# Kernel tuning notes

Measured on AMD Instinct MI355X. Metric: run time of the kernel, lower is better.

## Reference

```python
import jax, jax.numpy as jnp
import numpy as np

N_NODES = 100000
N_EDGES = 1600000
IN_CH = 128
OUT_CH = 64

def setup_inputs() -> dict:
    key = jax.random.key(0)
    k = jax.random.split(key, 7)
    x = jax.random.normal(k[0], (N_NODES, IN_CH), dtype=jnp.float32)
    edge_index = jax.random.randint(k[1], (2, N_EDGES), 0, N_NODES, dtype=jnp.int64)
    neg_edge_index = jax.random.randint(k[2], (2, N_EDGES), 0, N_NODES, dtype=jnp.int64)
    # GCNConv weight [in, out] + bias, Linear classifier [2*out, 2] + bias
    W = jax.random.normal(k[3], (IN_CH, OUT_CH), dtype=jnp.float32) / np.sqrt(IN_CH)
    b = jnp.zeros((OUT_CH,), dtype=jnp.float32)
    Wc = jax.random.normal(k[4], (2 * OUT_CH, 2), dtype=jnp.float32) / np.sqrt(2 * OUT_CH)
    bc = jnp.zeros((2,), dtype=jnp.float32)
    return {"x": x, "edge_index": edge_index, "neg_edge_index": neg_edge_index,
            "W": W, "b": b, "Wc": Wc, "bc": bc}

def reference(x, edge_index, neg_edge_index, W, b, Wc, bc):
    N = x.shape[0]
    # --- GCNConv: linear transform, add self-loops, symmetric deg normalization ---
    h = x @ W                                   # [N, out]
    loops = jnp.arange(N, dtype=edge_index.dtype)
    row = jnp.concatenate([edge_index[0], loops])   # source
    col = jnp.concatenate([edge_index[1], loops])   # target
    deg = jax.ops.segment_sum(jnp.ones(col.shape, h.dtype), col, num_segments=N)
    dinv = jnp.where(deg > 0, jax.lax.rsqrt(deg), 0.0)
    norm = dinv[row] * dinv[col]                # [E+N]
    agg = jax.ops.segment_sum(h[row] * norm[:, None], col, num_segments=N)
    z = jax.nn.relu(agg + b)                    # [N, out]
    # --- edge feature gather (pos + neg edges) + linear classifier ---
    total = jnp.concatenate([edge_index, neg_edge_index], axis=1)  # [2, 2E]
    feats = jnp.concatenate([z[total[0]], z[total[1]]], axis=1)    # [2E, 2*out]
    return feats @ Wc + bc                      # [2E, 2]
```

## Files before the change

### kernel.cpp

```cpp
#include <hip/hip_runtime.h>

#define IN_CH 128
#define OUT_CH 64
#define MAXBKT 256
#define BKT_SH 9
#define BKT_MSK 511
#define CAPB   9216
#define CAPB_PAD 16896
#define BINCHUNK 4096

typedef __attribute__((ext_vector_type(8))) short short8v;
typedef __attribute__((ext_vector_type(4))) float float4v;

union Pack { short8v s8; unsigned u[4]; };

__device__ __forceinline__ unsigned short f2bf(float f) {
    unsigned u = __float_as_uint(f);
    return (unsigned short)((u + 0x7fffu + ((u >> 16) & 1u)) >> 16);
}
__device__ __forceinline__ unsigned pk2(float a, float b) {
    return ((unsigned)f2bf(b) << 16) | (unsigned)f2bf(a);
}
__device__ __forceinline__ float bflo(unsigned d) { return __uint_as_float(d << 16); }
__device__ __forceinline__ float bfhi(unsigned d) { return __uint_as_float(d & 0xffff0000u); }

__global__ void k_zero_cnt(unsigned* __restrict__ cnt, int n) {
    int i = blockIdx.x * blockDim.x + threadIdx.x;
    if (i < n) cnt[i] = 0u;
}

__global__ __launch_bounds__(1024) void k_AG(const float* __restrict__ x,
                                             const float* __restrict__ W,
                                             const int* __restrict__ ei,
                                             unsigned* __restrict__ bucketCount,
                                             unsigned* __restrict__ binned,
                                             unsigned short* __restrict__ hs,
                                             int N, int E, int nbkt, int nBin) {
    __shared__ float smem[IN_CH * 66];
    int tid = threadIdx.x;

    if (blockIdx.x < nBin) {
        unsigned* hist = (unsigned*)smem;
        unsigned* resv = hist + MAXBKT;
        int start = blockIdx.x * BINCHUNK;
        int cnt = E - start; if (cnt > BINCHUNK) cnt = BINCHUNK;
        int i0 = tid * 4;

        if (tid < MAXBKT) hist[tid] = 0u;
        __syncthreads();

        if (i0 < cnt) {
            if (i0 + 4 <= cnt) {
                int4 c = ((const int4*)(ei + E + start))[tid];
                atomicAdd(&hist[c.x >> BKT_SH], 1u);
                atomicAdd(&hist[c.y >> BKT_SH], 1u);
                atomicAdd(&hist[c.z >> BKT_SH], 1u);
                atomicAdd(&hist[c.w >> BKT_SH], 1u);
            } else {
                for (int k = i0; k < cnt; ++k)
                    atomicAdd(&hist[ei[E + start + k] >> BKT_SH], 1u);
            }
        }
        __syncthreads();

        if (tid < nbkt) {
            resv[tid] = atomicAdd(&bucketCount[tid], hist[tid]);
            hist[tid] = 0u;
        }
        __syncthreads();

        if (i0 < cnt) {
            if (i0 + 4 <= cnt) {
                int4 c = ((const int4*)(ei + E + start))[tid];
                int4 r = ((const int4*)(ei + start))[tid];
                int cc[4] = {c.x, c.y, c.z, c.w};
                int rr[4] = {r.x, r.y, r.z, r.w};
#pragma unroll
                for (int k = 0; k < 4; ++k) {
                    int bkt = cc[k] >> BKT_SH;
                    unsigned rank = atomicAdd(&hist[bkt], 1u);
                    unsigned idx = resv[bkt] + rank;
                    if (idx < CAPB)
                        binned[(size_t)bkt * CAPB + idx] =
                            ((unsigned)rr[k] << BKT_SH) | (unsigned)(cc[k] & BKT_MSK);
                }
            } else {
                for (int k = i0; k < cnt; ++k) {
                    int c = ei[E + start + k];
                    int r = ei[start + k];
                    int bkt = c >> BKT_SH;
                    unsigned rank = atomicAdd(&hist[bkt], 1u);
                    unsigned idx = resv[bkt] + rank;
                    if (idx < CAPB)
                        binned[(size_t)bkt * CAPB + idx] =
                            ((unsigned)r << BKT_SH) | (unsigned)(c & BKT_MSK);
                }
            }
        }
    } else {
        int chunk = blockIdx.x - nBin;
        int wid = tid >> 6;
        int l   = tid & 63;
        int g   = l >> 4;
        int m   = l & 15;

        if (chunk == 0 && tid < 32)
            ((unsigned*)hs)[((size_t)N << 5) + tid] = 0u;

        float* Wl = smem;
        const float4* W4 = (const float4*)W;
#pragma unroll
        for (int j = 0; j < 2; ++j) {
            int i4 = tid + j * 1024;
            float4 w = W4[i4];
            int i = i4 * 4;
            int k = i >> 6, c = i & 63;
            float* dst = Wl + k * 66 + c;
            dst[0] = w.x; dst[1] = w.y; dst[2] = w.z; dst[3] = w.w;
        }
        __syncthreads();

        short8v bf[4][4];
#pragma unroll
        for (int s = 0; s < 4; ++s)
#pragma unroll
            for (int t = 0; t < 4; ++t) {
                Pack p;
#pragma unroll
                for (int jj = 0; jj < 4; ++jj) {
                    int k = s * 32 + g * 8 + 2 * jj;
                    float f0 = Wl[(k + 0) * 66 + t * 16 + m];
                    float f1 = Wl[(k + 1) * 66 + t * 16 + m];
                    p.u[jj] = pk2(f0, f1);
                }
                bf[s][t] = p.s8;
            }

        int R0 = chunk * 256 + wid * 16;
        int rowA = R0 + m; if (rowA > N - 1) rowA = N - 1;
        float4v acc[4];
#pragma unroll
        for (int t = 0; t < 4; ++t) acc[t] = (float4v){0.f, 0.f, 0.f, 0.f};

        const float4* x4 = (const float4*)x;
#pragma unroll
        for (int s = 0; s < 4; ++s) {
            const float4* ap = x4 + (size_t)rowA * 32 + s * 8 + g * 2;
            float4 a0 = ap[0];
            float4 a1 = ap[1];
            Pack pa;
            pa.u[0] = pk2(a0.x, a0.y);
            pa.u[1] = pk2(a0.z, a0.w);
            pa.u[2] = pk2(a1.x, a1.y);
            pa.u[3] = pk2(a1.z, a1.w);
#pragma unroll
            for (int t = 0; t < 4; ++t)
                acc[t] = __builtin_amdgcn_mfma_f32_16x16x32_bf16(pa.s8, bf[s][t], acc[t], 0, 0, 0);
        }

        int rbase = R0 + g * 4;
#pragma unroll
        for (int r = 0; r < 4; ++r) {
            int row = rbase + r;
            if (row < N) {
#pragma unroll
                for (int t = 0; t < 4; ++t)
                    hs[(size_t)row * OUT_CH + t * 16 + m] = f2bf(acc[t][r]);
            }
        }
    }
}

__global__ __launch_bounds__(1024) void k_csrB(const unsigned* __restrict__ binned,
                                               const unsigned* __restrict__ bucketCount,
                                               int* __restrict__ rows,
                                               unsigned* __restrict__ offs,
                                               unsigned* __restrict__ degPad,
                                               float* __restrict__ dinv,
                                               unsigned short* __restrict__ hs,
                                               int N, int nbkt) {
    __shared__ unsigned hist[512];
    __shared__ unsigned degS[512];
    __shared__ unsigned excl[512];
    __shared__ unsigned wsum[8];
    __shared__ unsigned wexc[8];
    __shared__ unsigned stage[CAPB];
    int tid = threadIdx.x;
    int b = blockIdx.x;
    unsigned cnt = bucketCount[b];
    if (cnt > (unsigned)CAPB) cnt = (unsigned)CAPB;
    size_t gbase = (size_t)b * CAPB_PAD;
    int nodeBase = b << BKT_SH;
    int nn = N - nodeBase; if (nn > 512) nn = 512;

    for (int i = tid; i < 512; i += 1024) hist[i] = 0u;
    __syncthreads();

    const unsigned* src = binned + (size_t)b * CAPB;
    for (unsigned i = tid; i < cnt; i += 1024) {
        unsigned p = src[i];
        stage[i] = p;
        atomicAdd(&hist[p & BKT_MSK], 1u);
    }
    __syncthreads();

    unsigned d = 0, dp = 0, winc = 0;
    if (tid < 512) {
        d = hist[tid];
        degS[tid] = d;
        dp = (d + 15u) & ~15u;
        winc = dp;
#pragma unroll
        for (int o = 1; o < 64; o <<= 1) {
            unsigned t = __shfl_up(winc, o);
            if ((tid & 63) >= o) winc += t;
        }
        if ((tid & 63) == 63) wsum[tid >> 6] = winc;
    }
    __syncthreads();
    if (tid < 8) {
        unsigned s = wsum[tid];
        unsigned inc = s;
#pragma unroll
        for (int o = 1; o < 8; o <<= 1) {
            unsigned t = __shfl_up(inc, o);
            if (tid >= o) inc += t;
        }
        wexc[tid] = inc - s;
    }
    __syncthreads();
    if (tid < 512) excl[tid] = wexc[tid >> 6] + winc - dp;
    __syncthreads();

    if (tid < nn) {
        offs[nodeBase + tid]   = (unsigned)gbase + excl[tid];
        degPad[nodeBase + tid] = dp;
        dinv[nodeBase + tid]   = rsqrtf((float)d + 1.0f);
    }

    for (unsigned i = tid; i < cnt; i += 1024) {
        unsigned p = stage[i];
        unsigned c = p & BKT_MSK;
        unsigned r = atomicAdd(&hist[c], 0xFFFFFFFFu);
        rows[gbase + excl[c] + r - 1u] = (int)(p >> BKT_SH);
    }
    if (tid < nn) {
        size_t base = gbase + excl[tid];
        for (unsigned p = d; p < dp; ++p) rows[base + p] = N;
    }

    int node_l = tid >> 1;
    if (node_l < nn) {
        float dv = rsqrtf((float)degS[node_l] + 1.0f);
        uint4* hq = (uint4*)hs;
        size_t base = ((size_t)(nodeBase + node_l) << 3) + ((size_t)(tid & 1) << 2);
#pragma unroll
        for (int q = 0; q < 4; ++q) {
            uint4 w = hq[base + q];
            w.x = pk2(bflo(w.x) * dv, bfhi(w.x) * dv);
            w.y = pk2(bflo(w.y) * dv, bfhi(w.y) * dv);
            w.z = pk2(bflo(w.z) * dv, bfhi(w.z) * dv);
            w.w = pk2(bflo(w.w) * dv, bfhi(w.w) * dv);
            hq[base + q] = w;
        }
    }
}

__global__ __launch_bounds__(256) void k_gather(const unsigned* __restrict__ offs,
                                                const unsigned* __restrict__ degPad,
                                                const int* __restrict__ rows,
                                                const unsigned* __restrict__ hsd,
                                                const float* __restrict__ dinv,
                                                const float* __restrict__ b,
                                                const float* __restrict__ Wc,
                                                float* __restrict__ u,
                                                float* __restrict__ v, int n) {
    int lane = threadIdx.x & 63;
    int half = lane >> 5;
    int l32  = lane & 31;
    int node = blockIdx.x * (blockDim.x >> 6) + (threadIdx.x >> 6);
    if (node >= n) return;
    unsigned start = offs[node];
    unsigned cntP = degPad[node];
    const int* rp = rows + start;

    unsigned ds = hsd[((size_t)node << 5) + l32];
    float acc0 = half ? 0.f : bflo(ds);
    float acc1 = half ? 0.f : bfhi(ds);

    for (unsigned j0 = 0; j0 < cntP; j0 += 64) {
        unsigned rem = cntP - j0;
        unsigned np = rem < 64u ? rem : 64u;
        int myidx = rp[j0 + (lane < (int)np ? lane : 0)];

        for (unsigned t0 = 0; t0 < np; t0 += 16) {
            int rr[8];
#pragma unroll
            for (int s = 0; s < 8; ++s)
                rr[s] = __shfl(myidx, (int)t0 + 2 * s + half);
            unsigned dd[8];
#pragma unroll
            for (int s = 0; s < 8; ++s)
                dd[s] = hsd[((size_t)rr[s] << 5) + l32];
#pragma unroll
            for (int s = 0; s < 8; ++s) {
                acc0 += bflo(dd[s]);
                acc1 += bfhi(dd[s]);
            }
        }
    }

    acc0 += __shfl_xor(acc0, 32);
    acc1 += __shfl_xor(acc1, 32);

    float di = dinv[node];
    float2 bv = ((const float2*)b)[l32];
    float z0 = fmaxf(fmaf(acc0, di, bv.x), 0.f);
    float z1 = fmaxf(fmaf(acc1, di, bv.y), 0.f);

    float4 w = ((const float4*)(Wc + (half ? 128 : 0)))[l32];
    float p0 = z0 * w.x + z1 * w.z;
    float p1 = z0 * w.y + z1 * w.w;
#pragma unroll
    for (int off = 16; off > 0; off >>= 1) {
        p0 += __shfl_xor(p0, off);
        p1 += __shfl_xor(p1, off);
    }
    float2 r; r.x = p0; r.y = p1;
    if (lane == 0)  ((float2*)u)[node] = r;
    if (lane == 32) ((float2*)v)[node] = r;
}

__global__ void k_edges(const int* __restrict__ ei, const int* __restrict__ nei,
                        const float* __restrict__ u, const float* __restrict__ v,
                        const float* __restrict__ bc, float* __restrict__ out, int E) {
    int i = blockIdx.x * blockDim.x + threadIdx.x;
    int quads = E >> 1;
    if (i >= quads) return;
    int halfQ = quads >> 1;
    const int* base = (i < halfQ) ? ei : nei;
    int pi = (i < halfQ) ? i : i - halfQ;
    int4 ss = ((const int4*)base)[pi];
    int4 dd = ((const int4*)(base + E))[pi];
    float2 u0 = ((const float2*)u)[ss.x];
    float2 u1 = ((const float2*)u)[ss.y];
    float2 u2 = ((const float2*)u)[ss.z];
    float2 u3 = ((const float2*)u)[ss.w];
    float2 v0 = ((const float2*)v)[dd.x];
    float2 v1 = ((const float2*)v)[dd.y];
    float2 v2 = ((const float2*)v)[dd.z];
    float2 v3 = ((const float2*)v)[dd.w];
    float b0 = bc[0], b1 = bc[1];
    float4 r0, r1;
    r0.x = u0.x + v0.x + b0;  r0.y = u0.y + v0.y + b1;
    r0.z = u1.x + v1.x + b0;  r0.w = u1.y + v1.y + b1;
    r1.x = u2.x + v2.x + b0;  r1.y = u2.y + v2.y + b1;
    r1.z = u3.x + v3.x + b0;  r1.w = u3.y + v3.y + b1;
    ((float4*)out)[2 * i + 0] = r0;
    ((float4*)out)[2 * i + 1] = r1;
}

extern "C" void kernel_launch(void* const* d_in, const int* in_sizes, int n_in,
                              void* d_out, int out_size, void* d_ws, size_t ws_size,
                              hipStream_t stream) {
    const float* x   = (const float*)d_in[0];
    const int*   ei  = (const int*)d_in[1];
    const int*   nei = (const int*)d_in[2];
    const float* W   = (const float*)d_in[3];
    const float* b   = (const float*)d_in[4];
    const float* Wc  = (const float*)d_in[5];
    const float* bc  = (const float*)d_in[6];
    float* out = (float*)d_out;

    const int N = in_sizes[0] / IN_CH;
    const int E = in_sizes[1] / 2;
    const int nbkt = (N + BKT_MSK) >> BKT_SH;
    const int nBin = (E + BINCHUNK - 1) / BINCHUNK;
    const int nG   = (N + 255) / 256;

    char* ws = (char*)d_ws;
    size_t off = 0;
    unsigned short* hs = (unsigned short*)(ws + off); off += ((size_t)N + 1) * OUT_CH * 2;
    unsigned* binned = (unsigned*)(ws + off); off += (size_t)MAXBKT * CAPB * 4;
    int*      rows   = (int*)(ws + off);      off += (size_t)MAXBKT * CAPB_PAD * 4;
    unsigned* offs   = (unsigned*)(ws + off); off += (size_t)N * 4;
    unsigned* degP   = (unsigned*)(ws + off); off += (size_t)N * 4;
    float*    dinv   = (float*)(ws + off);    off += (size_t)N * 4;
    float*    u      = (float*)(ws + off);    off += (size_t)N * 2 * 4;
    float*    v      = (float*)(ws + off);    off += (size_t)N * 2 * 4;
    unsigned* bucketCount = (unsigned*)(ws + off); off += (size_t)MAXBKT * 4;

    k_zero_cnt<<<1, 256, 0, stream>>>(bucketCount, MAXBKT);
    k_AG<<<nBin + nG, 1024, 0, stream>>>(x, W, ei, bucketCount, binned, hs, N, E, nbkt, nBin);
    k_csrB<<<nbkt, 1024, 0, stream>>>(binned, bucketCount, rows, offs, degP, dinv, hs, N, nbkt);
    k_gather<<<(N + 3) / 4, 256, 0, stream>>>(offs, degP, rows, (const unsigned*)hs, dinv, b, Wc, u, v, N);
    k_edges<<<(E / 2 + 255) / 256, 256, 0, stream>>>(ei, nei, u, v, bc, out, E);
}
```

Measured before the change: 131.6 us.

## Replace global atomic bucket reservation with histogram-scan-scatter binning

The edge binning is split into three passes. The first writes a per-chunk bucket histogram to a count matrix, a scan kernel computes exclusive offsets per bucket, and a scatter kernel writes the binned edges. This removes the global atomicAdd reservation and the zeroing kernel, and makes bucket placement deterministic. In exchange it adds two kernel launches and reads the edge columns a second time.

```diff
diff --git a/kernel.cpp b/kernel.cpp
--- a/kernel.cpp
+++ b/kernel.cpp
@@ -24,24 +24,17 @@
 __device__ __forceinline__ float bflo(unsigned d) { return __uint_as_float(d << 16); }
 __device__ __forceinline__ float bfhi(unsigned d) { return __uint_as_float(d & 0xffff0000u); }
 
-__global__ void k_zero_cnt(unsigned* __restrict__ cnt, int n) {
-    int i = blockIdx.x * blockDim.x + threadIdx.x;
-    if (i < n) cnt[i] = 0u;
-}
-
-__global__ __launch_bounds__(1024) void k_AG(const float* __restrict__ x,
-                                             const float* __restrict__ W,
-                                             const int* __restrict__ ei,
-                                             unsigned* __restrict__ bucketCount,
-                                             unsigned* __restrict__ binned,
-                                             unsigned short* __restrict__ hs,
-                                             int N, int E, int nbkt, int nBin) {
+__global__ __launch_bounds__(1024) void k_prepA(const float* __restrict__ x,
+                                                const float* __restrict__ W,
+                                                const int* __restrict__ ei,
+                                                unsigned* __restrict__ cnts,
+                                                unsigned short* __restrict__ hs,
+                                                int N, int E, int nbkt, int nBin) {
     __shared__ float smem[IN_CH * 66];
     int tid = threadIdx.x;
 
     if (blockIdx.x < nBin) {
         unsigned* hist = (unsigned*)smem;
-        unsigned* resv = hist + MAXBKT;
         int start = blockIdx.x * BINCHUNK;
         int cnt = E - start; if (cnt > BINCHUNK) cnt = BINCHUNK;
         int i0 = tid * 4;
@@ -63,40 +56,8 @@
         }
         __syncthreads();
 
-        if (tid < nbkt) {
-            resv[tid] = atomicAdd(&bucketCount[tid], hist[tid]);
-            hist[tid] = 0u;
-        }
-        __syncthreads();
-
-        if (i0 < cnt) {
-            if (i0 + 4 <= cnt) {
-                int4 c = ((const int4*)(ei + E + start))[tid];
-                int4 r = ((const int4*)(ei + start))[tid];
-                int cc[4] = {c.x, c.y, c.z, c.w};
-                int rr[4] = {r.x, r.y, r.z, r.w};
-#pragma unroll
-                for (int k = 0; k < 4; ++k) {
-                    int bkt = cc[k] >> BKT_SH;
-                    unsigned rank = atomicAdd(&hist[bkt], 1u);
-                    unsigned idx = resv[bkt] + rank;
-                    if (idx < CAPB)
-                        binned[(size_t)bkt * CAPB + idx] =
-                            ((unsigned)rr[k] << BKT_SH) | (unsigned)(cc[k] & BKT_MSK);
-                }
-            } else {
-                for (int k = i0; k < cnt; ++k) {
-                    int c = ei[E + start + k];
-                    int r = ei[start + k];
-                    int bkt = c >> BKT_SH;
-                    unsigned rank = atomicAdd(&hist[bkt], 1u);
-                    unsigned idx = resv[bkt] + rank;
-                    if (idx < CAPB)
-                        binned[(size_t)bkt * CAPB + idx] =
-                            ((unsigned)r << BKT_SH) | (unsigned)(c & BKT_MSK);
-                }
-            }
-        }
+        if (tid < nbkt)
+            cnts[(size_t)tid * nBin + blockIdx.x] = hist[tid];
     } else {
         int chunk = blockIdx.x - nBin;
         int wid = tid >> 6;
@@ -166,6 +127,85 @@
 #pragma unroll
                 for (int t = 0; t < 4; ++t)
                     hs[(size_t)row * OUT_CH + t * 16 + m] = f2bf(acc[t][r]);
+            }
+        }
+    }
+}
+
+__global__ __launch_bounds__(512) void k_scan(unsigned* __restrict__ cnts,
+                                              unsigned* __restrict__ bucketCount,
+                                              int nBin, int nbkt) {
+    __shared__ unsigned wsum[8];
+    __shared__ unsigned wexc[8];
+    int tid = threadIdx.x;
+    int k = blockIdx.x;
+    unsigned v = (tid < nBin) ? cnts[(size_t)k * nBin + tid] : 0u;
+    unsigned inc = v;
+#pragma unroll
+    for (int o = 1; o < 64; o <<= 1) {
+        unsigned t = __shfl_up(inc, o);
+        if ((tid & 63) >= o) inc += t;
+    }
+    if ((tid & 63) == 63) wsum[tid >> 6] = inc;
+    __syncthreads();
+    if (tid < 8) {
+        unsigned s = wsum[tid];
+        unsigned i2 = s;
+#pragma unroll
+        for (int o = 1; o < 8; o <<= 1) {
+            unsigned t = __shfl_up(i2, o);
+            if (tid >= o) i2 += t;
+        }
+        wexc[tid] = i2 - s;
+    }
+    __syncthreads();
+    unsigned excl = wexc[tid >> 6] + inc - v;
+    if (tid < nBin) cnts[(size_t)k * nBin + tid] = excl;
+    if (tid == nBin - 1) bucketCount[k] = excl + v;
+}
+
+__global__ __launch_bounds__(1024) void k_binC(const int* __restrict__ ei,
+                                               const unsigned* __restrict__ cnts,
+                                               unsigned* __restrict__ binned,
+                                               int E, int nbkt, int nBin) {
+    __shared__ unsigned hist[MAXBKT];
+    __shared__ unsigned base_l[MAXBKT];
+    int tid = threadIdx.x;
+    int start = blockIdx.x * BINCHUNK;
+    int cnt = E - start; if (cnt > BINCHUNK) cnt = BINCHUNK;
+    int i0 = tid * 4;
+
+    if (tid < MAXBKT) {
+        hist[tid] = 0u;
+        base_l[tid] = (tid < nbkt) ? cnts[(size_t)tid * nBin + blockIdx.x] : 0u;
+    }
+    __syncthreads();
+
+    if (i0 < cnt) {
+        if (i0 + 4 <= cnt) {
+            int4 c = ((const int4*)(ei + E + start))[tid];
+            int4 r = ((const int4*)(ei + start))[tid];
+            int cc[4] = {c.x, c.y, c.z, c.w};
+            int rr[4] = {r.x, r.y, r.z, r.w};
+#pragma unroll
+            for (int k = 0; k < 4; ++k) {
+                int bkt = cc[k] >> BKT_SH;
+                unsigned rank = atomicAdd(&hist[bkt], 1u);
+                unsigned idx = base_l[bkt] + rank;
+                if (idx < CAPB)
+                    binned[(size_t)bkt * CAPB + idx] =
+                        ((unsigned)rr[k] << BKT_SH) | (unsigned)(cc[k] & BKT_MSK);
+            }
+        } else {
+            for (int k = i0; k < cnt; ++k) {
+                int c = ei[E + start + k];
+                int r = ei[start + k];
+                int bkt = c >> BKT_SH;
+                unsigned rank = atomicAdd(&hist[bkt], 1u);
+                unsigned idx = base_l[bkt] + rank;
+                if (idx < CAPB)
+                    binned[(size_t)bkt * CAPB + idx] =
+                        ((unsigned)r << BKT_SH) | (unsigned)(c & BKT_MSK);
             }
         }
     }
@@ -389,9 +429,11 @@
     float*    u      = (float*)(ws + off);    off += (size_t)N * 2 * 4;
     float*    v      = (float*)(ws + off);    off += (size_t)N * 2 * 4;
     unsigned* bucketCount = (unsigned*)(ws + off); off += (size_t)MAXBKT * 4;
-
-    k_zero_cnt<<<1, 256, 0, stream>>>(bucketCount, MAXBKT);
-    k_AG<<<nBin + nG, 1024, 0, stream>>>(x, W, ei, bucketCount, binned, hs, N, E, nbkt, nBin);
+    unsigned* cnts   = (unsigned*)(ws + off); off += (size_t)MAXBKT * 512 * 4;
+
+    k_prepA<<<nBin + nG, 1024, 0, stream>>>(x, W, ei, cnts, hs, N, E, nbkt, nBin);
+    k_scan<<<nbkt, 512, 0, stream>>>(cnts, bucketCount, nBin, nbkt);
+    k_binC<<<nBin, 1024, 0, stream>>>(ei, cnts, binned, E, nbkt, nBin);
     k_csrB<<<nbkt, 1024, 0, stream>>>(binned, bucketCount, rows, offs, degP, dinv, hs, N, nbkt);
     k_gather<<<(N + 3) / 4, 256, 0, stream>>>(offs, degP, rows, (const unsigned*)hs, dinv, b, Wc, u, v, N);
     k_edges<<<(E / 2 + 255) / 256, 256, 0, stream>>>(ei, nei, u, v, bc, out, E);
```

Result: no change. 129.6 us (-1.4%).
